# Kernel optimization log

Hardware: AMD Instinct MI355X
Metric: run time of the kernel (lower is better)

Reference implementation:

```python
import jax, jax.numpy as jnp
import numpy as np

N_NODES = 100000
N_EDGES = 1600000
N_GRAPHS = 128
VOCAB = 10000
EMBED = 32
HID = 64
CLASSES = 2


def setup_inputs() -> dict:
    key = jax.random.key(0)
    ks = jax.random.split(key, 10)
    node_ids = jax.random.randint(ks[0], (N_NODES,), 0, VOCAB)
    edge_index = jax.random.randint(ks[1], (2, N_EDGES), 0, N_NODES)
    batch = jnp.sort(jax.random.randint(ks[2], (N_NODES,), 0, N_GRAPHS))
    s_e = 1.0 / np.sqrt(EMBED)
    s_h = 1.0 / np.sqrt(HID)
    return {
        "node_ids": node_ids,
        "edge_index": edge_index,
        "batch": batch,
        "embed_table": jax.random.normal(ks[3], (VOCAB, EMBED), jnp.float32),
        "W1_l": jax.random.normal(ks[4], (HID, EMBED), jnp.float32) * s_e,
        "W1_r": jax.random.normal(ks[5], (HID, EMBED), jnp.float32) * s_e,
        "b1": jnp.zeros((HID,), jnp.float32),
        "W2_l": jax.random.normal(ks[6], (HID, HID), jnp.float32) * s_h,
        "W2_r": jax.random.normal(ks[7], (HID, HID), jnp.float32) * s_h,
        "b2": jnp.zeros((HID,), jnp.float32),
        "W_lin": jax.random.normal(ks[8], (CLASSES, HID), jnp.float32) * s_h,
        "b_lin": jnp.zeros((CLASSES,), jnp.float32),
    }


def _sage_conv(x, src, dst, W_l, W_r, b):
    # mean-aggregate neighbor features: messages flow src -> dst
    msg_sum = jax.ops.segment_sum(x[src], dst, num_segments=x.shape[0])
    cnt = jax.ops.segment_sum(jnp.ones((src.shape[0], 1), x.dtype), dst,
                              num_segments=x.shape[0])
    mean = msg_sum / jnp.maximum(cnt, 1.0)
    return mean @ W_l.T + x @ W_r.T + b


def _global_mean_pool(x, batch, num_graphs):
    s = jax.ops.segment_sum(x, batch, num_segments=num_graphs)
    cnt = jax.ops.segment_sum(jnp.ones((x.shape[0], 1), x.dtype), batch,
                              num_segments=num_graphs)
    return s / jnp.maximum(cnt, 1.0)


def reference(node_ids, edge_index, batch, embed_table,
              W1_l, W1_r, b1, W2_l, W2_r, b2, W_lin, b_lin):
    src, dst = edge_index[0], edge_index[1]
    x = embed_table[node_ids]                       # [N, EMBED]
    x = jax.nn.relu(_sage_conv(x, src, dst, W1_l, W1_r, b1))  # [N, HID]
    x = jax.nn.relu(_sage_conv(x, src, dst, W2_l, W2_r, b2))  # [N, HID]
    g = _global_mean_pool(x, batch, N_GRAPHS)       # [G, HID]
    return g @ W_lin.T + b_lin                      # [G, CLASSES]
```

## Files before the change

kernel.cpp:

```cpp
#include <hip/hip_runtime.h>
#include <hip/hip_fp16.h>
#include <hip/hip_fp8.h>

#define N_NODES 100000
#define N_EDGES 1600000
#define N_GRAPHS 128
#define EMBED 32
#define HID 64
#define NBUCK 1563
#define CAP 1280
#define CHUNK 128
#define NGRP (N_EDGES / CHUNK)
#define PTILE 8192
#define NTILE ((N_EDGES + PTILE - 1) / PTILE)
#define TP 200
#define NPGRP 2048
#define PPER ((N_NODES + NPGRP - 1) / NPGRP)
#define EMB_BLK (N_NODES * 16 / 256)

typedef _Float16 f16x8 __attribute__((ext_vector_type(8)));
typedef float f32x4 __attribute__((ext_vector_type(4)));
typedef float f32x2 __attribute__((ext_vector_type(2)));
typedef unsigned short u16x8 __attribute__((ext_vector_type(8)));

__device__ __forceinline__ float fp8_to_f(unsigned char b) {
    __hip_fp8_e4m3 t; t.__x = (__hip_fp8_storage_t)b; return (float)t;
}
__device__ __forceinline__ unsigned char f_to_fp8(float f) {
    __hip_fp8_e4m3 t(f); return (unsigned char)t.__x;
}
__device__ __forceinline__ unsigned short h_bits(float f) {
    __half h = __float2half(f); return *(unsigned short*)&h;
}

#if defined(__has_builtin)
#if __has_builtin(__builtin_amdgcn_cvt_pk_f32_fp8)
#define HAVE_FP8_PK 1
#endif
#endif

__device__ __forceinline__ float2 fp8x2_to_f(unsigned short u) {
#ifdef HAVE_FP8_PK
    f32x2 r = __builtin_amdgcn_cvt_pk_f32_fp8((int)u, false);
    return make_float2(r[0], r[1]);
#else
    return make_float2(fp8_to_f((unsigned char)(u & 0xFF)),
                       fp8_to_f((unsigned char)(u >> 8)));
#endif
}

__global__ __launch_bounds__(256)
void k_stage1(const int* __restrict__ ids, const float* __restrict__ table,
              __half2* __restrict__ x0h, uchar2* __restrict__ x0q,
              const int* __restrict__ dst, int* __restrict__ htile,
              float* __restrict__ zf, int* __restrict__ idf) {
    __shared__ int hist[NBUCK];
    int tid = threadIdx.x, b = blockIdx.x;
    if (b < EMB_BLK) {
        int gid = b * 256 + tid;
        int n = gid >> 4, q = gid & 15;
        int id = ids[n];
        float2 t = ((const float2*)(table + (size_t)id * EMBED))[q];
        x0h[(size_t)n * 16 + q] = __floats2half2_rn(t.x, t.y);
        x0q[(size_t)n * 16 + q] = make_uchar2(f_to_fp8(t.x), f_to_fp8(t.y));
        return;
    }
    if (b < EMB_BLK + NTILE) {
        int t = b - EMB_BLK;
        int e0 = t * PTILE;
        int cnt = min(PTILE, N_EDGES - e0);
        for (int i = tid; i < NBUCK; i += 256) hist[i] = 0;
        __syncthreads();
        for (int i = tid; i < cnt; i += 256)
            atomicAdd(&hist[dst[e0 + i] >> 6], 1);
        __syncthreads();
        for (int bb = tid; bb < NBUCK; bb += 256)
            htile[bb * TP + t] = hist[bb];
        return;
    }
    for (int i = tid; i < 64 * N_GRAPHS + N_GRAPHS; i += 256) zf[i] = 0.f;
    for (int i = tid; i < 2 * NGRP; i += 256) idf[i] = -1;
}

__global__ __launch_bounds__(256)
void k_scanB(int* __restrict__ htile, int* __restrict__ bcnt) {
    int wv = threadIdx.x >> 6, lane = threadIdx.x & 63;
    int b = blockIdx.x * 4 + wv;
    if (b >= NBUCK) return;
    int* row = htile + b * TP;
    int v[4]; int s = 0;
    #pragma unroll
    for (int i = 0; i < 4; ++i) {
        int t = lane * 4 + i;
        v[i] = (t < NTILE) ? row[t] : 0;
        s += v[i];
    }
    int inc = s;
    for (int d = 1; d < 64; d <<= 1) {
        int u = __shfl_up(inc, d);
        if (lane >= d) inc += u;
    }
    int run = inc - s;
    #pragma unroll
    for (int i = 0; i < 4; ++i) {
        int t = lane * 4 + i;
        if (t < NTILE) row[t] = run;
        run += v[i];
    }
    int total = __shfl(inc, 63);
    if (lane == 0) bcnt[b] = total;
}

__global__ __launch_bounds__(1024)
void k_bscan(const int* __restrict__ bcnt, int* __restrict__ bbase,
             int* __restrict__ off_total) {
    __shared__ int leaf[1024];
    int t = threadIdx.x;
    int i0 = 2 * t, i1 = 2 * t + 1;
    int a = (i0 < NBUCK) ? bcnt[i0] : 0;
    int b = (i1 < NBUCK) ? bcnt[i1] : 0;
    leaf[t] = a + b;
    __syncthreads();
    for (int d = 1; d < 1024; d <<= 1) {
        int v = (t >= d) ? leaf[t - d] : 0;
        __syncthreads();
        leaf[t] += v;
        __syncthreads();
    }
    int excl = leaf[t] - (a + b);
    if (i0 < NBUCK) bbase[i0] = excl;
    if (i1 < NBUCK) bbase[i1] = excl + a;
    if (t == 1023) off_total[0] = leaf[1023];
}

__global__ __launch_bounds__(256)
void k_scatC(const int* __restrict__ src, const int* __restrict__ dst,
             const int* __restrict__ htile, const int* __restrict__ bbase,
             int* __restrict__ epk) {
    __shared__ int cur[NBUCK];
    int orig = blockIdx.x;
    int xcd = orig & 7, idx = orig >> 3;
    const int q = NTILE >> 3, r = NTILE & 7;
    int t = (xcd < r ? xcd * (q + 1) : r * (q + 1) + (xcd - r) * q) + idx;
    int tid = threadIdx.x;
    int e0 = t * PTILE;
    int cnt = min(PTILE, N_EDGES - e0);
    for (int b = tid; b < NBUCK; b += 256)
        cur[b] = htile[b * TP + t] + bbase[b];
    __syncthreads();
    for (int i = tid; i < cnt; i += 256) {
        int d = dst[e0 + i];
        int s = src[e0 + i];
        int b = d >> 6;
        int pos = atomicAdd(&cur[b], 1);
        epk[pos] = s | ((d & 63) << 17);
    }
}

__global__ __launch_bounds__(256)
void k_sortb(const int* __restrict__ bcnt, const int* __restrict__ epk,
             const int* __restrict__ bbase,
             int* __restrict__ ssrc, int* __restrict__ deg, int* __restrict__ off) {
    __shared__ int hist4[4][64];
    __shared__ int loff[64];
    __shared__ int cur4[4][64];
    int tid = threadIdx.x, bkt = blockIdx.x;
    int w = tid >> 6, lane = tid & 63;
    int base = bbase[bkt];
    int cntE = min(bcnt[bkt], CAP);
    hist4[w][lane] = 0;
    __syncthreads();
    const int* eb = epk + base;
    int v[5]; bool have[5];
    #pragma unroll
    for (int qq = 0; qq < 5; ++qq) {
        int i = qq * 256 + tid;
        have[qq] = (i < cntE);
        if (have[qq]) {
            v[qq] = eb[i];
            atomicAdd(&hist4[w][v[qq] >> 17], 1);
        }
    }
    __syncthreads();
    if (tid < 64) {
        int h0 = hist4[0][tid], h1 = hist4[1][tid];
        int h2 = hist4[2][tid], h3 = hist4[3][tid];
        int h = h0 + h1 + h2 + h3;
        int inc = h;
        for (int d = 1; d < 64; d <<= 1) {
            int u = __shfl_up(inc, d);
            if (tid >= d) inc += u;
        }
        int excl = inc - h;
        loff[tid] = excl;
        cur4[0][tid] = excl;
        cur4[1][tid] = excl + h0;
        cur4[2][tid] = excl + h0 + h1;
        cur4[3][tid] = excl + h0 + h1 + h2;
        int n0 = bkt << 6;
        if (n0 + tid < N_NODES) {
            deg[n0 + tid] = h;
            off[n0 + tid] = base + excl;
        }
    }
    __syncthreads();
    #pragma unroll
    for (int qq = 0; qq < 5; ++qq) {
        if (have[qq]) {
            int l = v[qq] >> 17;
            int pos = atomicAdd(&cur4[w][l], 1);
            ssrc[base + pos] = v[qq] & 0x1FFFF;
        }
    }
}

template<int L>
__global__ __launch_bounds__(256)
void k_agg(const int* __restrict__ ssrc, const int* __restrict__ off,
           const unsigned short* __restrict__ featq,
           float2* __restrict__ agg,
           float2* __restrict__ carry,
           int* __restrict__ carry_id)
{
    int tid = blockIdx.x * 256 + threadIdx.x;
    int grp = tid / L;
    int lane = tid % L;
    if (grp >= NGRP) return;
    int base = grp * CHUNK;
    int end  = base + CHUNK;
    int lo = 0, hi = N_NODES - 1;
    while (lo < hi) {
        int mid = (lo + hi + 1) >> 1;
        if (off[mid] <= base) lo = mid; else hi = mid - 1;
    }
    int d = lo;
    bool head = (off[d] >= base);
    int next = off[d + 1];
    float2 acc = make_float2(0.f, 0.f);
    for (int j = base; j < end; j += 8) {
        int4 pa = ((const int4*)(ssrc + j))[0];
        int4 pb = ((const int4*)(ssrc + j))[1];
        int ss[8] = {pa.x, pa.y, pa.z, pa.w, pb.x, pb.y, pb.z, pb.w};
        unsigned short v[8];
        #pragma unroll
        for (int q = 0; q < 8; ++q)
            v[q] = featq[(size_t)ss[q] * L + lane];
        #pragma unroll
        for (int q = 0; q < 8; ++q) {
            int jj = j + q;
            if (jj >= next) {
                if (head) {
                    agg[d * L + lane] = acc;
                } else {
                    carry[grp * L + lane] = acc;
                    if (lane == 0) carry_id[grp] = d;
                }
                acc = make_float2(0.f, 0.f);
                head = true;
                d++;
                while (off[d + 1] <= jj) d++;
                next = off[d + 1];
            }
            float2 f = fp8x2_to_f(v[q]);
            acc.x += f.x;
            acc.y += f.y;
        }
    }
    if (head) {
        agg[d * L + lane] = acc;
    } else {
        carry[grp * L + lane] = acc;
        if (lane == 0) carry_id[grp] = d;
    }
}

template<int L>
__global__ __launch_bounds__(256)
void k_fix(const float2* __restrict__ carry, const int* __restrict__ carry_id,
           float2* __restrict__ agg) {
    int tid = blockIdx.x * 256 + threadIdx.x;
    int grp = tid / L;
    int lane = tid % L;
    if (grp >= NGRP) return;
    int d = carry_id[grp];
    if (d < 0) return;
    float2 c = carry[grp * L + lane];
    unsafeAtomicAdd(&((float*)agg)[(d * L + lane) * 2],     c.x);
    unsafeAtomicAdd(&((float*)agg)[(d * L + lane) * 2 + 1], c.y);
}

template<int CIN, bool WQ8>
__global__ __launch_bounds__(256)
void k_updmm(const float* __restrict__ agg, const int* __restrict__ deg,
             const __half* __restrict__ own,
             const float* __restrict__ Wl, const float* __restrict__ Wr,
             const float* __restrict__ bias,
             __half* __restrict__ outh, unsigned char* __restrict__ outq) {
    constexpr int K = 2 * CIN;
    constexpr int C8 = K / 8;
    constexpr int ST = K + 8;
    __shared__ alignas(16) unsigned short catL[64 * ST];
    __shared__ alignas(16) unsigned short WLds[64 * ST];
    __shared__ float invL[64];
    int tid = threadIdx.x;
    int n0 = blockIdx.x * 64;
    int nn = min(64, N_NODES - n0);
    if (tid < 64) {
        int dg = (tid < nn) ? deg[n0 + tid] : 0;
        invL[tid] = (dg > 0) ? 1.0f / (float)dg : 0.0f;
    }
    for (int idx = tid; idx < 64 * C8; idx += 256) {
        int o = idx / C8, k = (idx % C8) * 8;
        const float* wsrc = (k < CIN) ? (Wl + o * CIN + k) : (Wr + o * CIN + k - CIN);
        float4 a = ((const float4*)wsrc)[0];
        float4 b = ((const float4*)wsrc)[1];
        u16x8 h = {h_bits(a.x), h_bits(a.y), h_bits(a.z), h_bits(a.w),
                   h_bits(b.x), h_bits(b.y), h_bits(b.z), h_bits(b.w)};
        *(u16x8*)&WLds[o * ST + k] = h;
    }
    __syncthreads();
    for (int idx = tid; idx < 64 * C8; idx += 256) {
        int n = idx / C8, k = (idx % C8) * 8;
        u16x8 h = {0, 0, 0, 0, 0, 0, 0, 0};
        if (n < nn) {
            if (k < CIN) {
                const float* as = agg + (size_t)(n0 + n) * CIN + k;
                float4 a = ((const float4*)as)[0];
                float4 b = ((const float4*)as)[1];
                float iv = invL[n];
                h = (u16x8){h_bits(a.x * iv), h_bits(a.y * iv),
                            h_bits(a.z * iv), h_bits(a.w * iv),
                            h_bits(b.x * iv), h_bits(b.y * iv),
                            h_bits(b.z * iv), h_bits(b.w * iv)};
            } else {
                h = *(const u16x8*)(own + (size_t)(n0 + n) * CIN + (k - CIN));
            }
        }
        *(u16x8*)&catL[n * ST + k] = h;
    }
    __syncthreads();
    int w = tid >> 6, lane = tid & 63;
    int nb = w * 16;
    if (nb >= nn) return;
    int col = lane & 15, g = lane >> 4;
    f16x8 aF[K / 32];
    #pragma unroll
    for (int ks = 0; ks < K / 32; ++ks)
        aF[ks] = *(const f16x8*)&catL[(nb + col) * ST + ks * 32 + g * 8];
    #pragma unroll
    for (int nt = 0; nt < 4; ++nt) {
        f32x4 c = {0.f, 0.f, 0.f, 0.f};
        #pragma unroll
        for (int ks = 0; ks < K / 32; ++ks) {
            f16x8 bF = *(const f16x8*)&WLds[(nt * 16 + col) * ST + ks * 32 + g * 8];
            c = __builtin_amdgcn_mfma_f32_16x16x32_f16(aF[ks], bF, c, 0, 0, 0);
        }
        int o = nt * 16 + col;
        float bo = bias[o];
        #pragma unroll
        for (int r = 0; r < 4; ++r) {
            int n = nb + g * 4 + r;
            if (n < nn) {
                float v = fmaxf(c[r] + bo, 0.f);
                outh[(size_t)(n0 + n) * HID + o] = __float2half(v);
                if constexpr (WQ8)
                    outq[(size_t)(n0 + n) * HID + o] = f_to_fp8(v);
            }
        }
    }
}

__global__ __launch_bounds__(256)
void k_pool_part(const __half* __restrict__ h2h, const int* __restrict__ batch,
                 float* __restrict__ pooled, float* __restrict__ gcnt) {
    int grp = blockIdx.x * 4 + (threadIdx.x >> 6);
    int lane = threadIdx.x & 63;
    int start = grp * PPER;
    if (start >= N_NODES) return;
    int end = start + PPER; if (end > N_NODES) end = N_NODES;
    float acc = 0.0f, c = 0.0f;
    int cur = batch[start];
    for (int n = start; n < end; ++n) {
        int bb = batch[n];
        if (bb != cur) {
            unsafeAtomicAdd(&pooled[cur * HID + lane], acc);
            if (lane == 0) unsafeAtomicAdd(&gcnt[cur], c);
            acc = 0.0f; c = 0.0f; cur = bb;
        }
        acc += __half2float(h2h[(size_t)n * HID + lane]);
        c += 1.0f;
    }
    unsafeAtomicAdd(&pooled[cur * HID + lane], acc);
    if (lane == 0) unsafeAtomicAdd(&gcnt[cur], c);
}

__global__ __launch_bounds__(256)
void k_final(const float* __restrict__ pooled, const float* __restrict__ gcnt,
             const float* __restrict__ W_lin, const float* __restrict__ b_lin,
             float* __restrict__ out) {
    int t = threadIdx.x;
    int g = t >> 1, c = t & 1;
    float inv = 1.0f / fmaxf(gcnt[g], 1.0f);
    float sum = b_lin[c];
    #pragma unroll 8
    for (int k = 0; k < HID; ++k)
        sum += pooled[g * HID + k] * inv * W_lin[c * HID + k];
    out[g * 2 + c] = sum;
}

extern "C" void kernel_launch(void* const* d_in, const int* in_sizes, int n_in,
                              void* d_out, int out_size, void* d_ws, size_t ws_size,
                              hipStream_t stream) {
    const int*   node_ids = (const int*)d_in[0];
    const int*   ei       = (const int*)d_in[1];
    const int*   batch    = (const int*)d_in[2];
    const float* table    = (const float*)d_in[3];
    const float* W1l      = (const float*)d_in[4];
    const float* W1r      = (const float*)d_in[5];
    const float* b1       = (const float*)d_in[6];
    const float* W2l      = (const float*)d_in[7];
    const float* W2r      = (const float*)d_in[8];
    const float* b2       = (const float*)d_in[9];
    const float* Wlin     = (const float*)d_in[10];
    const float* blin     = (const float*)d_in[11];
    const int* src = ei;
    const int* dst = ei + N_EDGES;

    int*   bcnt   = (int*)d_ws;
    float* pooled = (float*)(bcnt + 1600);
    float* gcnt   = pooled + 64 * N_GRAPHS;
    int* id16  = (int*)(gcnt + N_GRAPHS);
    int* id32  = id16 + NGRP;
    int* bbase = id32 + NGRP;
    int* ideg  = bbase + 1600;
    int* ioff  = ideg + N_NODES;
    int* htile = ioff + N_NODES + 1;
    int* epk   = htile + (size_t)NBUCK * TP;
    int* issrc = epk + N_EDGES;
    size_t int_total = 1600 + 8192 + 128 + NGRP + NGRP + 1600 + N_NODES
                     + (N_NODES + 1) + (size_t)NBUCK * TP + N_EDGES + N_EDGES;
    size_t falign = (int_total + 3) & ~(size_t)3;
    float*  aggAB = (float*)d_ws + falign;
    float2* c16   = (float2*)(aggAB + 64 * N_NODES);
    float2* c32   = (float2*)((float*)c16 + NGRP * 32);
    __half2* x0h  = (__half2*)((float*)c32 + NGRP * 64);
    __half*  h1h  = (__half*)(x0h + 16 * N_NODES);
    __half*  h2h  = h1h + 64 * N_NODES;
    uchar2*  x0q  = (uchar2*)(h2h + 64 * N_NODES);
    unsigned char* h1q = (unsigned char*)(x0q + 16 * N_NODES);

    k_stage1<<<EMB_BLK + NTILE + 1, 256, 0, stream>>>(node_ids, table, x0h, x0q,
                                                      dst, htile, pooled, id16);
    k_scanB<<<(NBUCK + 3) / 4, 256, 0, stream>>>(htile, bcnt);
    k_bscan<<<1, 1024, 0, stream>>>(bcnt, bbase, ioff + N_NODES);
    k_scatC<<<NTILE, 256, 0, stream>>>(src, dst, htile, bbase, epk);
    k_sortb<<<NBUCK, 256, 0, stream>>>(bcnt, epk, bbase, issrc, ideg, ioff);

    k_agg<16><<<(NGRP * 16 + 255) / 256, 256, 0, stream>>>(
        issrc, ioff, (const unsigned short*)x0q, (float2*)aggAB, c16, id16);
    k_fix<16><<<(NGRP * 16 + 255) / 256, 256, 0, stream>>>(c16, id16, (float2*)aggAB);
    k_updmm<EMBED, true><<<(N_NODES + 63) / 64, 256, 0, stream>>>(
        aggAB, ideg, (const __half*)x0h, W1l, W1r, b1, h1h, h1q);

    k_agg<32><<<(NGRP * 32 + 255) / 256, 256, 0, stream>>>(
        issrc, ioff, (const unsigned short*)h1q, (float2*)aggAB, c32, id32);
    k_fix<32><<<(NGRP * 32 + 255) / 256, 256, 0, stream>>>(c32, id32, (float2*)aggAB);
    k_updmm<HID, false><<<(N_NODES + 63) / 64, 256, 0, stream>>>(
        aggAB, ideg, h1h, W2l, W2r, b2, h2h, nullptr);

    k_pool_part<<<NPGRP / 4, 256, 0, stream>>>(h2h, batch, pooled, gcnt);
    k_final<<<1, 256, 0, stream>>>(pooled, gcnt, Wlin, blin, (float*)d_out);
}
```

Before: 198.9 us.

## Fuse global mean pooling into second SAGE update matmul kernel

The layer-2 update kernel now stages its ReLU output tile in shared memory and performs the per-graph segmented sum there, issuing atomics into the pooled buffer directly. This removes the h2h fp16 intermediate write and readback and one kernel launch. In exchange there are many more pooling atomics, roughly one set per 16-node slice instead of per 49-node group, plus extra block syncs in the matmul kernel.

```diff
diff --git a/kernel.cpp b/kernel.cpp
--- a/kernel.cpp
+++ b/kernel.cpp
@@ -14,8 +14,6 @@
 #define PTILE 8192
 #define NTILE ((N_EDGES + PTILE - 1) / PTILE)
 #define TP 200
-#define NPGRP 2048
-#define PPER ((N_NODES + NPGRP - 1) / NPGRP)
 #define EMB_BLK (N_NODES * 16 / 256)
 
 typedef _Float16 f16x8 __attribute__((ext_vector_type(8)));
@@ -289,13 +287,15 @@
     unsafeAtomicAdd(&((float*)agg)[(d * L + lane) * 2 + 1], c.y);
 }
 
-template<int CIN, bool WQ8>
+template<int CIN, bool WQ8, bool POOL>
 __global__ __launch_bounds__(256)
 void k_updmm(const float* __restrict__ agg, const int* __restrict__ deg,
              const __half* __restrict__ own,
              const float* __restrict__ Wl, const float* __restrict__ Wr,
              const float* __restrict__ bias,
-             __half* __restrict__ outh, unsigned char* __restrict__ outq) {
+             __half* __restrict__ outh, unsigned char* __restrict__ outq,
+             const int* __restrict__ batch,
+             float* __restrict__ pooled, float* __restrict__ gcnt) {
     constexpr int K = 2 * CIN;
     constexpr int C8 = K / 8;
     constexpr int ST = K + 8;
@@ -341,57 +341,78 @@
     __syncthreads();
     int w = tid >> 6, lane = tid & 63;
     int nb = w * 16;
-    if (nb >= nn) return;
+    bool active = (nb < nn);
     int col = lane & 15, g = lane >> 4;
-    f16x8 aF[K / 32];
-    #pragma unroll
-    for (int ks = 0; ks < K / 32; ++ks)
-        aF[ks] = *(const f16x8*)&catL[(nb + col) * ST + ks * 32 + g * 8];
-    #pragma unroll
-    for (int nt = 0; nt < 4; ++nt) {
-        f32x4 c = {0.f, 0.f, 0.f, 0.f};
+    f32x4 cacc[4];
+    if (active) {
+        f16x8 aF[K / 32];
         #pragma unroll
-        for (int ks = 0; ks < K / 32; ++ks) {
-            f16x8 bF = *(const f16x8*)&WLds[(nt * 16 + col) * ST + ks * 32 + g * 8];
-            c = __builtin_amdgcn_mfma_f32_16x16x32_f16(aF[ks], bF, c, 0, 0, 0);
-        }
-        int o = nt * 16 + col;
-        float bo = bias[o];
+        for (int ks = 0; ks < K / 32; ++ks)
+            aF[ks] = *(const f16x8*)&catL[(nb + col) * ST + ks * 32 + g * 8];
         #pragma unroll
-        for (int r = 0; r < 4; ++r) {
-            int n = nb + g * 4 + r;
-            if (n < nn) {
-                float v = fmaxf(c[r] + bo, 0.f);
-                outh[(size_t)(n0 + n) * HID + o] = __float2half(v);
-                if constexpr (WQ8)
-                    outq[(size_t)(n0 + n) * HID + o] = f_to_fp8(v);
-            }
-        }
-    }
-}
-
-__global__ __launch_bounds__(256)
-void k_pool_part(const __half* __restrict__ h2h, const int* __restrict__ batch,
-                 float* __restrict__ pooled, float* __restrict__ gcnt) {
-    int grp = blockIdx.x * 4 + (threadIdx.x >> 6);
-    int lane = threadIdx.x & 63;
-    int start = grp * PPER;
-    if (start >= N_NODES) return;
-    int end = start + PPER; if (end > N_NODES) end = N_NODES;
-    float acc = 0.0f, c = 0.0f;
-    int cur = batch[start];
-    for (int n = start; n < end; ++n) {
-        int bb = batch[n];
-        if (bb != cur) {
+        for (int nt = 0; nt < 4; ++nt) {
+            f32x4 c = {0.f, 0.f, 0.f, 0.f};
+            #pragma unroll
+            for (int ks = 0; ks < K / 32; ++ks) {
+                f16x8 bF = *(const f16x8*)&WLds[(nt * 16 + col) * ST + ks * 32 + g * 8];
+                c = __builtin_amdgcn_mfma_f32_16x16x32_f16(aF[ks], bF, c, 0, 0, 0);
+            }
+            cacc[nt] = c;
+        }
+    }
+    if constexpr (!POOL) {
+        if (!active) return;
+        #pragma unroll
+        for (int nt = 0; nt < 4; ++nt) {
+            int o = nt * 16 + col;
+            float bo = bias[o];
+            #pragma unroll
+            for (int r = 0; r < 4; ++r) {
+                int n = nb + g * 4 + r;
+                if (n < nn) {
+                    float v = fmaxf(cacc[nt][r] + bo, 0.f);
+                    outh[(size_t)(n0 + n) * HID + o] = __float2half(v);
+                    if constexpr (WQ8)
+                        outq[(size_t)(n0 + n) * HID + o] = f_to_fp8(v);
+                }
+            }
+        }
+    } else {
+        __syncthreads();
+        float* pf = (float*)catL;
+        if (active) {
+            #pragma unroll
+            for (int nt = 0; nt < 4; ++nt) {
+                int o = nt * 16 + col;
+                float bo = bias[o];
+                #pragma unroll
+                for (int r = 0; r < 4; ++r) {
+                    int n = nb + g * 4 + r;
+                    if (n < nn)
+                        pf[n * 64 + o] = fmaxf(cacc[nt][r] + bo, 0.f);
+                }
+            }
+        }
+        __syncthreads();
+        int start = w * 16;
+        int end = min(start + 16, nn);
+        if (start < end) {
+            float acc = 0.f, c = 0.f;
+            int cur = batch[n0 + start];
+            for (int n = start; n < end; ++n) {
+                int bb = batch[n0 + n];
+                if (bb != cur) {
+                    unsafeAtomicAdd(&pooled[cur * HID + lane], acc);
+                    if (lane == 0) unsafeAtomicAdd(&gcnt[cur], c);
+                    acc = 0.f; c = 0.f; cur = bb;
+                }
+                acc += pf[n * 64 + lane];
+                c += 1.f;
+            }
             unsafeAtomicAdd(&pooled[cur * HID + lane], acc);
             if (lane == 0) unsafeAtomicAdd(&gcnt[cur], c);
-            acc = 0.0f; c = 0.0f; cur = bb;
-        }
-        acc += __half2float(h2h[(size_t)n * HID + lane]);
-        c += 1.0f;
-    }
-    unsafeAtomicAdd(&pooled[cur * HID + lane], acc);
-    if (lane == 0) unsafeAtomicAdd(&gcnt[cur], c);
+        }
+    }
 }
 
 __global__ __launch_bounds__(256)
@@ -445,8 +466,7 @@
     float2* c32   = (float2*)((float*)c16 + NGRP * 32);
     __half2* x0h  = (__half2*)((float*)c32 + NGRP * 64);
     __half*  h1h  = (__half*)(x0h + 16 * N_NODES);
-    __half*  h2h  = h1h + 64 * N_NODES;
-    uchar2*  x0q  = (uchar2*)(h2h + 64 * N_NODES);
+    uchar2*  x0q  = (uchar2*)(h1h + 64 * N_NODES);
     unsigned char* h1q = (unsigned char*)(x0q + 16 * N_NODES);
 
     k_stage1<<<EMB_BLK + NTILE + 1, 256, 0, stream>>>(node_ids, table, x0h, x0q,
@@ -459,15 +479,16 @@
     k_agg<16><<<(NGRP * 16 + 255) / 256, 256, 0, stream>>>(
         issrc, ioff, (const unsigned short*)x0q, (float2*)aggAB, c16, id16);
     k_fix<16><<<(NGRP * 16 + 255) / 256, 256, 0, stream>>>(c16, id16, (float2*)aggAB);
-    k_updmm<EMBED, true><<<(N_NODES + 63) / 64, 256, 0, stream>>>(
-        aggAB, ideg, (const __half*)x0h, W1l, W1r, b1, h1h, h1q);
+    k_updmm<EMBED, true, false><<<(N_NODES + 63) / 64, 256, 0, stream>>>(
+        aggAB, ideg, (const __half*)x0h, W1l, W1r, b1, h1h, h1q,
+        nullptr, nullptr, nullptr);
 
     k_agg<32><<<(NGRP * 32 + 255) / 256, 256, 0, stream>>>(
         issrc, ioff, (const unsigned short*)h1q, (float2*)aggAB, c32, id32);
     k_fix<32><<<(NGRP * 32 + 255) / 256, 256, 0, stream>>>(c32, id32, (float2*)aggAB);
-    k_updmm<HID, false><<<(N_NODES + 63) / 64, 256, 0, stream>>>(
-        aggAB, ideg, h1h, W2l, W2r, b2, h2h, nullptr);
-
-    k_pool_part<<<NPGRP / 4, 256, 0, stream>>>(h2h, batch, pooled, gcnt);
+    k_updmm<HID, false, true><<<(N_NODES + 63) / 64, 256, 0, stream>>>(
+        aggAB, ideg, h1h, W2l, W2r, b2, nullptr, nullptr,
+        batch, pooled, gcnt);
+
     k_final<<<1, 256, 0, stream>>>(pooled, gcnt, Wlin, blin, (float*)d_out);
 }
```

Measured after the change: 199.9 us. No clear change (+0.5%).
